# Optimization experiments

Measured on AMD Instinct MI355X. Metric: run time of the kernel, lower is better.

The kernel has to match this reference:

```python
import jax, jax.numpy as jnp
import numpy as np

N, D, H = 8192, 1280, 16
K = D // H          # head_dim = 80
S = 16              # number of packed segments
L = N // S          # tokens per segment = 512
SCALE = K ** -0.5


def rotate_half(x):
    x1, x2 = jnp.split(x, 2, axis=-1)
    return jnp.concatenate([-x2, x1], axis=-1)


def setup_inputs() -> dict:
    key = jax.random.key(0)
    ks = jax.random.split(key, 4)
    # RoPE tables over head_dim, shared by all heads
    inv_freq = 1.0 / (10000.0 ** (jnp.arange(0, K, 2, dtype=jnp.float32) / K))
    freqs = jnp.outer(jnp.arange(N, dtype=jnp.float32), inv_freq)  # [N, K/2]
    emb = jnp.concatenate([freqs, freqs], axis=-1)                 # [N, K]
    return {
        "hidden_ND": jax.random.normal(ks[0], (N, D), jnp.float32),
        "cu_seqlens": jnp.arange(S + 1, dtype=jnp.int32) * L,      # equal-length segments
        "cos_NK": jnp.cos(emb),
        "sin_NK": jnp.sin(emb),
        "qkv_w": jax.random.normal(ks[1], (D, 3 * D), jnp.float32) * (D ** -0.5),
        "qkv_b": jnp.zeros((3 * D,), jnp.float32),
        "proj_w": jax.random.normal(ks[2], (D, D), jnp.float32) * (D ** -0.5),
        "proj_b": jnp.zeros((D,), jnp.float32),
    }


def reference(hidden_ND, cu_seqlens, cos_NK, sin_NK, qkv_w, qkv_b, proj_w, proj_b):
    n = hidden_ND.shape[0]
    qkv = (hidden_ND @ qkv_w + qkv_b).reshape(n, 3, H, K)
    q, k, v = qkv[:, 0], qkv[:, 1], qkv[:, 2]          # each [N, H, K]
    cos = cos_NK[:, None, :]
    sin = sin_NK[:, None, :]
    q = q * cos + rotate_half(q) * sin
    k = k * cos + rotate_half(k) * sin
    # Block-diagonal attention over equal-length segments defined by cu_seqlens.
    num_seqs = cu_seqlens.shape[0] - 1
    seg_len = n // num_seqs
    qs = q.reshape(num_seqs, seg_len, H, K)
    ks_ = k.reshape(num_seqs, seg_len, H, K)
    vs = v.reshape(num_seqs, seg_len, H, K)
    logits = jnp.einsum('slhk,smhk->shlm', qs, ks_) * SCALE   # [S, H, L, L]
    w = jax.nn.softmax(logits.astype(jnp.float32), axis=-1).astype(logits.dtype)
    out = jnp.einsum('shlm,smhk->slhk', w, vs).reshape(n, H * K)
    return out @ proj_w + proj_b
```

## Files before the change

### kernel.cpp

```cpp
#include <hip/hip_runtime.h>

#define LOG2E 1.44269504088896340736f
#define ATT_SCALE 0.11180339887498949f

typedef _Float16 half8 __attribute__((ext_vector_type(8)));
typedef _Float16 half4v __attribute__((ext_vector_type(4)));
typedef __fp16 fp16x2 __attribute__((ext_vector_type(2)));
typedef float f32x4 __attribute__((ext_vector_type(4)));

#define MFMA(a, b, c) __builtin_amdgcn_mfma_f32_16x16x32_f16((a), (b), (c), 0, 0, 0)

__device__ __forceinline__ void async16(const _Float16* g, _Float16* l) {
  __builtin_amdgcn_global_load_lds(
      (const __attribute__((address_space(1))) unsigned int*)g,
      (__attribute__((address_space(3))) unsigned int*)l,
      16, 0, 0);
}

#define FENCE() asm volatile("" ::: "memory")
#define PH_MID()                                         \
  do {                                                   \
    FENCE();                                             \
    __builtin_amdgcn_s_barrier();                        \
    asm volatile("s_waitcnt lgkmcnt(0)" ::: "memory");   \
    __builtin_amdgcn_sched_barrier(0);                   \
  } while (0)
#define PH_END()                                         \
  do {                                                   \
    __builtin_amdgcn_sched_barrier(0);                   \
    FENCE();                                             \
    __builtin_amdgcn_s_barrier();                        \
    FENCE();                                             \
  } while (0)

__global__ __launch_bounds__(256) void cvt_k(const float* __restrict__ in,
                                             _Float16* __restrict__ out, int n4) {
  int i = blockIdx.x * 256 + threadIdx.x;
  if (i < n4) {
    f32x4 v = ((const f32x4*)in)[i];
    half4v hv;
    hv[0] = (_Float16)v[0]; hv[1] = (_Float16)v[1];
    hv[2] = (_Float16)v[2]; hv[3] = (_Float16)v[3];
    ((half4v*)out)[i] = hv;
  }
}

__global__ __launch_bounds__(256) void transpose_cvt_k(const float* __restrict__ in,
                                                       _Float16* __restrict__ out,
                                                       int R, int C) {
  __shared__ float tile[32][33];
  const int tx = threadIdx.x & 31, ty = threadIdx.x >> 5;
  const int c0 = blockIdx.x * 32, r0 = blockIdx.y * 32;
#pragma unroll
  for (int i = 0; i < 32; i += 8)
    tile[ty + i][tx] = in[(size_t)(r0 + ty + i) * C + c0 + tx];
  __syncthreads();
#pragma unroll
  for (int i = 0; i < 32; i += 8)
    out[(size_t)(c0 + ty + i) * R + r0 + tx] = (_Float16)tile[tx][ty + i];
}

__global__ __launch_bounds__(512, 2) void gemm256_k(const _Float16* __restrict__ A,
                                                    const _Float16* __restrict__ BT,
                                                    const float* __restrict__ bias,
                                                    _Float16* __restrict__ Qf,
                                                    _Float16* __restrict__ Kf,
                                                    _Float16* __restrict__ VTf) {
  __shared__ _Float16 sA[2][2][128 * 64];
  __shared__ _Float16 sB[2][2][128 * 64];
  const int tid = threadIdx.x;
  const int wave = tid >> 6, lane = tid & 63;
  const int quad = lane >> 4, l16 = lane & 15;
  const int wm = wave >> 2, wn = wave & 3;
  const int bh = wn >> 1, brb = (wn & 1) * 64;
  const int KD = 1280, NT = 20;

  const int id = blockIdx.x;
  const int xcd = id & 7;
  const int qq = (id >> 3) & 3;
  const int tn = id >> 5;
  const int tm = xcd * 4 + qq;
  const int m0 = tm * 256, n0 = tn * 256;

  f32x4 acc[8][4] = {};

  auto stageA = [&](int buf, int half, int kt) {
#pragma unroll
    for (int c = 0; c < 2; ++c) {
      const int s = c * 512 + wave * 64 + lane;
      const int row = s >> 3;
      const int lg = (s & 7) ^ (row & 7);
      async16(A + (size_t)(m0 + half * 128 + row) * KD + kt * 64 + lg * 8,
              &sA[buf][half][(size_t)(c * 512 + wave * 64) * 8]);
    }
  };
  auto stageB = [&](int buf, int half, int kt) {
#pragma unroll
    for (int c = 0; c < 2; ++c) {
      const int s = c * 512 + wave * 64 + lane;
      const int row = s >> 3;
      const int lg = (s & 7) ^ (row & 7);
      async16(BT + (size_t)(n0 + half * 128 + row) * KD + kt * 64 + lg * 8,
              &sB[buf][half][(size_t)(c * 512 + wave * 64) * 8]);
    }
  };
  auto ldA = [&](half8* af, const _Float16* hp, int rh) {
#pragma unroll
    for (int i = 0; i < 4; ++i)
#pragma unroll
      for (int kk = 0; kk < 2; ++kk) {
        const int lrow = rh * 64 + i * 16 + l16;
        const int pg = (kk * 4 + quad) ^ (l16 & 7);
        af[i * 2 + kk] = *(const half8*)(hp + lrow * 64 + pg * 8);
      }
  };
  auto ldB = [&](half8* bf, const _Float16* hp, int ch) {
#pragma unroll
    for (int j = 0; j < 2; ++j)
#pragma unroll
      for (int kk = 0; kk < 2; ++kk) {
        const int brow = brb + ch * 32 + j * 16 + l16;
        const int pg = (kk * 4 + quad) ^ (l16 & 7);
        bf[j * 2 + kk] = *(const half8*)(hp + brow * 64 + pg * 8);
      }
  };
  auto mmaq = [&](int r, int c, const half8* af, const half8* bf) {
#pragma unroll
    for (int i = 0; i < 4; ++i)
#pragma unroll
      for (int j = 0; j < 2; ++j)
#pragma unroll
        for (int kk = 0; kk < 2; ++kk)
          acc[r * 4 + i][c * 2 + j] =
              MFMA(af[i * 2 + kk], bf[j * 2 + kk], acc[r * 4 + i][c * 2 + j]);
  };

  stageA(0, 0, 0); stageA(0, 1, 0);
  stageB(0, 0, 0); stageB(0, 1, 0);
  stageB(1, 0, 1); stageB(1, 1, 1);
  asm volatile("s_waitcnt vmcnt(4)" ::: "memory");
  __builtin_amdgcn_s_barrier();
  FENCE();

  half8 af[8], bf0[4], bf1[4];
#pragma unroll 2
  for (int t = 0; t < NT; ++t) {
    const int buf = t & 1;
    const _Float16* aH = sA[buf][wm];
    const _Float16* bH = sB[buf][bh];

    ldA(af, aH, 0);
    ldB(bf0, bH, 0);
    if (t + 1 < NT) stageA(buf ^ 1, 0, t + 1);
    PH_MID();
    __builtin_amdgcn_s_setprio(1);
    mmaq(0, 0, af, bf0);
    __builtin_amdgcn_s_setprio(0);
    PH_END();

    ldB(bf1, bH, 1);
    if (t + 1 < NT) stageA(buf ^ 1, 1, t + 1);
    PH_MID();
    __builtin_amdgcn_s_setprio(1);
    mmaq(0, 1, af, bf1);
    __builtin_amdgcn_s_setprio(0);
    PH_END();

    ldA(af, aH, 1);
    if (t + 2 < NT) stageB(buf, 0, t + 2);
    PH_MID();
    __builtin_amdgcn_s_setprio(1);
    mmaq(1, 1, af, bf1);
    __builtin_amdgcn_s_setprio(0);
    PH_END();

    if (t + 2 < NT) stageB(buf, 1, t + 2);
    if (t == NT - 2)
      asm volatile("s_waitcnt vmcnt(0)" ::: "memory");
    else if (t < NT - 2)
      asm volatile("s_waitcnt vmcnt(4)" ::: "memory");
    PH_MID();
    __builtin_amdgcn_s_setprio(1);
    mmaq(1, 0, af, bf0);
    __builtin_amdgcn_s_setprio(0);
    PH_END();
  }

#pragma unroll
  for (int ridx = 0; ridx < 8; ++ridx) {
#pragma unroll
    for (int cidx = 0; cidx < 4; ++cidx) {
      const int col = n0 + wn * 64 + cidx * 16 + l16;
      const float bv = bias[col];
      const int rowb = m0 + wm * 128 + ridx * 16 + quad * 4;
      const int which = col / 1280;
      const int rem = col - which * 1280;
      const int h = rem / 80;
      const int kk = rem - h * 80;
#pragma unroll
      for (int r = 0; r < 4; ++r) {
        const float v = acc[ridx][cidx][r] + bv;
        const int mrow = rowb + r;
        const int s = mrow >> 9, l = mrow & 511;
        const int shh = s * 16 + h;
        if (which == 0)
          Qf[((size_t)shh * 512 + l) * 96 + kk] = (_Float16)v;
        else if (which == 1)
          Kf[((size_t)shh * 512 + l) * 96 + kk] = (_Float16)v;
        else
          VTf[((size_t)shh * 80 + kk) * 512 + l] = (_Float16)v;
      }
    }
  }
}

__global__ __launch_bounds__(256) void gemm_k(const _Float16* __restrict__ A,
                                              const _Float16* __restrict__ BT,
                                              const float* __restrict__ bias,
                                              float* __restrict__ Out) {
  __shared__ _Float16 sA[128 * 32];
  __shared__ _Float16 sB[128 * 32];
  const int tid = threadIdx.x;
  const int wave = tid >> 6, lane = tid & 63;
  const int quad = lane >> 4, l16 = lane & 15;
  const int m0 = blockIdx.x * 128;
  const int n0 = blockIdx.y * 128;
  const int mw = (wave & 1) * 64, nw = (wave >> 1) * 64;
  const int KD = 1280;

  const int srcg = (lane & 3) ^ ((lane >> 3) & 3);
  const int rg = (quad ^ ((l16 >> 1) & 3)) * 8;

  f32x4 acc[4][4] = {};

  for (int kt = 0; kt < KD; kt += 32) {
#pragma unroll
    for (int c = 0; c < 2; ++c) {
      const int j = wave * 2 + c;
      const int row = j * 16 + (lane >> 2);
      async16(A + (size_t)(m0 + row) * KD + kt + srcg * 8, &sA[j * 512]);
      async16(BT + (size_t)(n0 + row) * KD + kt + srcg * 8, &sB[j * 512]);
    }
    __syncthreads();
    half8 af[4], bf[4];
#pragma unroll
    for (int i = 0; i < 4; ++i) {
      af[i] = *(const half8*)&sA[(mw + i * 16 + l16) * 32 + rg];
      bf[i] = *(const half8*)&sB[(nw + i * 16 + l16) * 32 + rg];
    }
#pragma unroll
    for (int i = 0; i < 4; ++i)
#pragma unroll
      for (int j2 = 0; j2 < 4; ++j2)
        acc[i][j2] = MFMA(af[i], bf[j2], acc[i][j2]);
    __syncthreads();
  }

#pragma unroll
  for (int i = 0; i < 4; ++i) {
#pragma unroll
    for (int j2 = 0; j2 < 4; ++j2) {
      const int col = n0 + nw + j2 * 16 + l16;
      const float bv = bias[col];
      const int rowb = m0 + mw + i * 16 + quad * 4;
#pragma unroll
      for (int r = 0; r < 4; ++r)
        Out[(size_t)(rowb + r) * 1280 + col] = acc[i][j2][r] + bv;
    }
  }
}

__global__ __launch_bounds__(256) void rope_k(_Float16* __restrict__ Qf,
                                              _Float16* __restrict__ Kf,
                                              const float* __restrict__ cosNK,
                                              const float* __restrict__ sinNK) {
  const int gid = blockIdx.x * 256 + threadIdx.x;
  const int j = gid & 63;
  const int row = gid >> 6;
  const int qk = row >> 17;
  const int r = row & 131071;
  _Float16* buf = qk ? Kf : Qf;
  const int l = r & 511;
  const int s = r >> 13;
  const int t = s * 512 + l;
  const size_t base = (size_t)r * 96;
  if (j < 40) {
    const float v1 = (float)buf[base + j];
    const float v2 = (float)buf[base + j + 40];
    const float c1 = cosNK[t * 80 + j], s1 = sinNK[t * 80 + j];
    const float c2 = cosNK[t * 80 + j + 40], s2 = sinNK[t * 80 + j + 40];
    buf[base + j] = (_Float16)(v1 * c1 - v2 * s1);
    buf[base + j + 40] = (_Float16)(v2 * c2 + v1 * s2);
  } else if (j < 56) {
    buf[base + 40 + j] = (_Float16)0.f;
  }
}

__global__ __launch_bounds__(256) void attn_k(const _Float16* __restrict__ Qf,
                                              const _Float16* __restrict__ Kf,
                                              const _Float16* __restrict__ VTf,
                                              _Float16* __restrict__ attnA) {
  __shared__ _Float16 sP[128 * 72];
  __shared__ _Float16 sK[64 * 104];
  __shared__ _Float16 sV[96 * 72];
  const int tid = threadIdx.x;
  const int wave = tid >> 6, lane = tid & 63;
  const int quad = lane >> 4, l16 = lane & 15;
  const int shh = blockIdx.x;
  const int qt = blockIdx.y;
  const int h = shh & 15;
  const int s = shh >> 4;

  const _Float16* Qb = Qf + ((size_t)shh * 512 + qt * 128) * 96;
  const _Float16* Kb0 = Kf + (size_t)shh * 512 * 96;
  const _Float16* Vb0 = VTf + (size_t)shh * 80 * 512;

  const _Float16 c1h = (_Float16)(ATT_SCALE * LOG2E);
  half8 qf[2][3];
#pragma unroll
  for (int rt = 0; rt < 2; ++rt)
#pragma unroll
    for (int ks = 0; ks < 3; ++ks) {
      half8 t = *(const half8*)(Qb + (size_t)(wave * 32 + rt * 16 + l16) * 96 +
                                ks * 32 + quad * 8);
#pragma unroll
      for (int e = 0; e < 8; ++e) t[e] *= c1h;
      qf[rt][ks] = t;
    }

  for (int idx = tid; idx < 16 * 72; idx += 256) sV[80 * 72 + idx] = (_Float16)1.f;

  f32x4 o[2][6] = {};

  for (int kc = 0; kc < 8; ++kc) {
    __syncthreads();
    const _Float16* Kb = Kb0 + (size_t)kc * 64 * 96;
#pragma unroll
    for (int c = 0; c < 4; ++c) {
      const int j = wave + 4 * c;
      if (j < 13) {
        const int off = j * 1024 + lane * 16;
        const int krow = off / 208;
        const int kcol = off - krow * 208;
        if (kcol < 192)
          async16(Kb + (size_t)krow * 96 + (kcol >> 1), &sK[j * 512]);
      }
    }
#pragma unroll
    for (int c = 0; c < 3; ++c) {
      const int j = wave + 4 * c;
      const int off = j * 1024 + lane * 16;
      const int vrow = off / 144;
      const int colb = off - vrow * 144;
      if (vrow < 80 && colb < 128)
        async16(Vb0 + (size_t)vrow * 512 + kc * 64 + (colb >> 1), &sV[j * 512]);
    }
    __syncthreads();

    f32x4 sacc[2][4] = {};
#pragma unroll
    for (int mt = 0; mt < 4; ++mt) {
#pragma unroll
      for (int ks = 0; ks < 3; ++ks) {
        half8 kb = *(const half8*)&sK[(mt * 16 + l16) * 104 + ks * 32 + quad * 8];
        sacc[0][mt] = MFMA(kb, qf[0][ks], sacc[0][mt]);
        sacc[1][mt] = MFMA(kb, qf[1][ks], sacc[1][mt]);
      }
    }

#pragma unroll
    for (int rt = 0; rt < 2; ++rt) {
#pragma unroll
      for (int mt = 0; mt < 4; ++mt) {
        union { fp16x2 h2[2]; half4v h4; } u;
        u.h2[0] = __builtin_amdgcn_cvt_pkrtz(
            __builtin_amdgcn_exp2f(sacc[rt][mt][0]),
            __builtin_amdgcn_exp2f(sacc[rt][mt][1]));
        u.h2[1] = __builtin_amdgcn_cvt_pkrtz(
            __builtin_amdgcn_exp2f(sacc[rt][mt][2]),
            __builtin_amdgcn_exp2f(sacc[rt][mt][3]));
        *(half4v*)&sP[(wave * 32 + rt * 16 + l16) * 72 + mt * 16 + quad * 4] = u.h4;
      }
    }

#pragma unroll
    for (int ks = 0; ks < 2; ++ks) {
      half8 pa[2];
      pa[0] = *(const half8*)&sP[(wave * 32 + 0 + l16) * 72 + ks * 32 + quad * 8];
      pa[1] = *(const half8*)&sP[(wave * 32 + 16 + l16) * 72 + ks * 32 + quad * 8];
#pragma unroll
      for (int ft = 0; ft < 6; ++ft) {
        half8 vb = *(const half8*)&sV[(ft * 16 + l16) * 72 + ks * 32 + quad * 8];
        o[0][ft] = MFMA(pa[0], vb, o[0][ft]);
        o[1][ft] = MFMA(pa[1], vb, o[1][ft]);
      }
    }
  }

#pragma unroll
  for (int rt = 0; rt < 2; ++rt) {
#pragma unroll
    for (int r = 0; r < 4; ++r) {
      const float inv = 1.0f / o[rt][5][r];
      const int token = s * 512 + qt * 128 + wave * 32 + rt * 16 + quad * 4 + r;
#pragma unroll
      for (int ft = 0; ft < 5; ++ft)
        attnA[(size_t)token * 1280 + h * 80 + ft * 16 + l16] =
            (_Float16)(o[rt][ft][r] * inv);
    }
  }
}

extern "C" void kernel_launch(void* const* d_in, const int* in_sizes, int n_in,
                              void* d_out, int out_size, void* d_ws, size_t ws_size,
                              hipStream_t stream) {
  (void)in_sizes; (void)n_in; (void)out_size; (void)ws_size;
  const float* hidden = (const float*)d_in[0];
  const float* cosNK = (const float*)d_in[2];
  const float* sinNK = (const float*)d_in[3];
  const float* qkv_w = (const float*)d_in[4];
  const float* qkv_b = (const float*)d_in[5];
  const float* proj_w = (const float*)d_in[6];
  const float* proj_b = (const float*)d_in[7];
  float* out = (float*)d_out;

  char* ws = (char*)d_ws;
  _Float16* hA    = (_Float16*)(ws);
  _Float16* wT    = (_Float16*)(ws + 20971520);
  _Float16* projT = (_Float16*)(ws + 30801920);
  _Float16* Qf    = (_Float16*)(ws + 34078720);
  _Float16* Kf    = (_Float16*)(ws + 59244544);
  _Float16* VTf   = (_Float16*)(ws + 84410368);
  _Float16* attnA = (_Float16*)(ws + 105381888);

  cvt_k<<<10240, 256, 0, stream>>>(hidden, hA, 2621440);
  transpose_cvt_k<<<dim3(120, 40), 256, 0, stream>>>(qkv_w, wT, 1280, 3840);
  transpose_cvt_k<<<dim3(40, 40), 256, 0, stream>>>(proj_w, projT, 1280, 1280);
  gemm256_k<<<480, 512, 0, stream>>>(hA, wT, qkv_b, Qf, Kf, VTf);
  rope_k<<<65536, 256, 0, stream>>>(Qf, Kf, cosNK, sinNK);
  attn_k<<<dim3(256, 4), 256, 0, stream>>>(Qf, Kf, VTf, attnA);
  gemm_k<<<dim3(64, 10), 256, 0, stream>>>(attnA, projT, proj_b, out);
}
```

Measured before the change: 354.0 us.

## Software-pipeline LDS fragment loads across phases with single barrier per phase

Restructures the QKV GEMM main loop so LDS fragment reads for the next phase or next k-tile are issued before the current MFMA block, with double-buffered A/B register fragments. This replaces the two-barrier-plus-lgkmcnt(0) pattern with one barrier per phase. Global-to-LDS staging is merged into full-tile issues (four async loads per call instead of two halves). The aim is to hide LDS latency behind MFMAs and cut barrier count. In exchange it raises register pressure, and the looser wait ordering risks LDS read/write hazards.

```diff
diff --git a/kernel.cpp b/kernel.cpp
--- a/kernel.cpp
+++ b/kernel.cpp
@@ -18,19 +18,13 @@
 }
 
 #define FENCE() asm volatile("" ::: "memory")
-#define PH_MID()                                         \
-  do {                                                   \
-    FENCE();                                             \
-    __builtin_amdgcn_s_barrier();                        \
-    asm volatile("s_waitcnt lgkmcnt(0)" ::: "memory");   \
-    __builtin_amdgcn_sched_barrier(0);                   \
-  } while (0)
-#define PH_END()                                         \
-  do {                                                   \
-    __builtin_amdgcn_sched_barrier(0);                   \
-    FENCE();                                             \
-    __builtin_amdgcn_s_barrier();                        \
-    FENCE();                                             \
+#define PHB()                                   \
+  do {                                          \
+    __builtin_amdgcn_sched_barrier(0);          \
+    FENCE();                                    \
+    __builtin_amdgcn_s_barrier();               \
+    FENCE();                                    \
+    __builtin_amdgcn_sched_barrier(0);          \
   } while (0)
 
 __global__ __launch_bounds__(256) void cvt_k(const float* __restrict__ in,
@@ -84,24 +78,24 @@
 
   f32x4 acc[8][4] = {};
 
-  auto stageA = [&](int buf, int half, int kt) {
-#pragma unroll
-    for (int c = 0; c < 2; ++c) {
+  auto stageA2 = [&](int buf, int kt) {
+#pragma unroll
+    for (int c = 0; c < 4; ++c) {
       const int s = c * 512 + wave * 64 + lane;
       const int row = s >> 3;
       const int lg = (s & 7) ^ (row & 7);
-      async16(A + (size_t)(m0 + half * 128 + row) * KD + kt * 64 + lg * 8,
-              &sA[buf][half][(size_t)(c * 512 + wave * 64) * 8]);
-    }
-  };
-  auto stageB = [&](int buf, int half, int kt) {
-#pragma unroll
-    for (int c = 0; c < 2; ++c) {
+      async16(A + (size_t)(m0 + row) * KD + kt * 64 + lg * 8,
+              &sA[buf][0][(size_t)(c * 512 + wave * 64) * 8]);
+    }
+  };
+  auto stageB2 = [&](int buf, int kt) {
+#pragma unroll
+    for (int c = 0; c < 4; ++c) {
       const int s = c * 512 + wave * 64 + lane;
       const int row = s >> 3;
       const int lg = (s & 7) ^ (row & 7);
-      async16(BT + (size_t)(n0 + half * 128 + row) * KD + kt * 64 + lg * 8,
-              &sB[buf][half][(size_t)(c * 512 + wave * 64) * 8]);
+      async16(BT + (size_t)(n0 + row) * KD + kt * 64 + lg * 8,
+              &sB[buf][0][(size_t)(c * 512 + wave * 64) * 8]);
     }
   };
   auto ldA = [&](half8* af, const _Float16* hp, int rh) {
@@ -114,7 +108,7 @@
         af[i * 2 + kk] = *(const half8*)(hp + lrow * 64 + pg * 8);
       }
   };
-  auto ldB = [&](half8* bf, const _Float16* hp, int ch) {
+  auto ldBh = [&](half8* bf, const _Float16* hp, int ch) {
 #pragma unroll
     for (int j = 0; j < 2; ++j)
 #pragma unroll
@@ -135,55 +129,66 @@
               MFMA(af[i * 2 + kk], bf[j * 2 + kk], acc[r * 4 + i][c * 2 + j]);
   };
 
-  stageA(0, 0, 0); stageA(0, 1, 0);
-  stageB(0, 0, 0); stageB(0, 1, 0);
-  stageB(1, 0, 1); stageB(1, 1, 1);
+  const _Float16* aP[2] = {&sA[0][wm][0], &sA[1][wm][0]};
+  const _Float16* bP[2] = {&sB[0][bh][0], &sB[1][bh][0]};
+
+  stageA2(0, 0);
+  stageB2(0, 0);
+  stageB2(1, 1);
   asm volatile("s_waitcnt vmcnt(4)" ::: "memory");
   __builtin_amdgcn_s_barrier();
   FENCE();
-
-  half8 af[8], bf0[4], bf1[4];
-#pragma unroll 2
-  for (int t = 0; t < NT; ++t) {
-    const int buf = t & 1;
-    const _Float16* aH = sA[buf][wm];
-    const _Float16* bH = sB[buf][bh];
-
-    ldA(af, aH, 0);
-    ldB(bf0, bH, 0);
-    if (t + 1 < NT) stageA(buf ^ 1, 0, t + 1);
-    PH_MID();
+  __builtin_amdgcn_sched_barrier(0);
+
+  half8 afA[8], afB[8], bf0a[4], bf0b[4], bf1[4];
+  ldA(afA, aP[0], 0);
+  ldBh(bf0a, bP[0], 0);
+
+  auto tile = [&](int t, int buf, half8* bf0c, half8* bf0n) {
+    const _Float16* aH = aP[buf];
+    const _Float16* bH = bP[buf];
+
+    PHB();
+    if (t + 1 < NT) stageA2(buf ^ 1, t + 1);
+    ldBh(bf1, bH, 1);
+    __builtin_amdgcn_sched_barrier(0);
     __builtin_amdgcn_s_setprio(1);
-    mmaq(0, 0, af, bf0);
+    mmaq(0, 0, afA, bf0c);
     __builtin_amdgcn_s_setprio(0);
-    PH_END();
-
-    ldB(bf1, bH, 1);
-    if (t + 1 < NT) stageA(buf ^ 1, 1, t + 1);
-    PH_MID();
+
+    PHB();
+    ldA(afB, aH, 1);
+    __builtin_amdgcn_sched_barrier(0);
     __builtin_amdgcn_s_setprio(1);
-    mmaq(0, 1, af, bf1);
+    mmaq(0, 1, afA, bf1);
     __builtin_amdgcn_s_setprio(0);
-    PH_END();
-
-    ldA(af, aH, 1);
-    if (t + 2 < NT) stageB(buf, 0, t + 2);
-    PH_MID();
+
+    PHB();
+    if (t + 2 < NT) stageB2(buf, t + 2);
+    __builtin_amdgcn_sched_barrier(0);
     __builtin_amdgcn_s_setprio(1);
-    mmaq(1, 1, af, bf1);
+    mmaq(1, 1, afB, bf1);
     __builtin_amdgcn_s_setprio(0);
-    PH_END();
-
-    if (t + 2 < NT) stageB(buf, 1, t + 2);
-    if (t == NT - 2)
+    __builtin_amdgcn_sched_barrier(0);
+    if (t < NT - 2)
+      asm volatile("s_waitcnt vmcnt(4)" ::: "memory");
+    else if (t == NT - 2)
       asm volatile("s_waitcnt vmcnt(0)" ::: "memory");
-    else if (t < NT - 2)
-      asm volatile("s_waitcnt vmcnt(4)" ::: "memory");
-    PH_MID();
+
+    PHB();
+    if (t + 1 < NT) {
+      ldA(afA, aP[buf ^ 1], 0);
+      ldBh(bf0n, bP[buf ^ 1], 0);
+    }
+    __builtin_amdgcn_sched_barrier(0);
     __builtin_amdgcn_s_setprio(1);
-    mmaq(1, 0, af, bf0);
+    mmaq(1, 0, afB, bf0c);
     __builtin_amdgcn_s_setprio(0);
-    PH_END();
+  };
+
+  for (int t2 = 0; t2 < NT; t2 += 2) {
+    tile(t2, 0, bf0a, bf0b);
+    tile(t2 + 1, 1, bf0b, bf0a);
   }
 
 #pragma unroll
```

New measurement: 423.7 us. 19.7% more time.
